# Kernel tuning notes

Hardware: AMD Instinct MI355X
Metric: run time of the kernel (lower is better)

## Reference

```python
import jax, jax.numpy as jnp
import numpy as np

N, M = 4096, 256

def setup_inputs() -> dict:
    key = jax.random.key(0)
    k1, k2 = jax.random.split(key)
    y_pred = jax.random.normal(k1, (N, M), dtype=jnp.float32)
    y = jax.random.normal(k2, (N, 1), dtype=jnp.float32)
    return {"y_pred": y_pred, "y": y}

def reference(y_pred, y):
    n, m = y_pred.shape
    # MAE term: mean(|y_pred - y|), y broadcast over ensemble dim
    mae_loss = jnp.mean(jnp.abs(y_pred - y))
    # Ensemble spread term: sum_{i,k,l} |x[i,k] - x[i,l]| / (n * 2 * m^2)
    # pairwise diffs: [n, m, m]
    pair = jnp.abs(y_pred[:, None, :] - y_pred[:, :, None])
    mix_loss = jnp.sum(pair) / (n * 2 * m ** 2)
    return mae_loss - mix_loss
```

## Files before the change

### kernel.cpp

```cpp
#include <hip/hip_runtime.h>


constexpr int N_ROWS = 4096;
constexpr int M_COLS = 256;
constexpr int ROWS_PER_BLOCK = 4;

__global__ __launch_bounds__(256)
void crps_kernel(const float* __restrict__ y_pred,
                 const float* __restrict__ y,
                 float* __restrict__ out) {
    __shared__ __align__(16) float4 rows[ROWS_PER_BLOCK][M_COLS / 4];
    __shared__ float wsum[ROWS_PER_BLOCK];

    const int wave = threadIdx.x >> 6;
    const int lane = threadIdx.x & 63;
    const int row  = blockIdx.x * ROWS_PER_BLOCK + wave;

    const float4* gp = reinterpret_cast<const float4*>(y_pred + row * M_COLS);
    const float4 xk = gp[lane];
    rows[wave][lane] = xk;
    const float yi = y[row];
    __syncthreads();

    float m0 = 0.0f, m1 = 0.0f, m2 = 0.0f, m3 = 0.0f;
    const float4* r4 = rows[wave];
    #pragma unroll 8
    for (int l = 0; l < M_COLS / 4; ++l) {
        const float4 v = r4[l];
        m0 += fabsf(xk.x - v.x) + fabsf(xk.x - v.y) + fabsf(xk.x - v.z) + fabsf(xk.x - v.w);
        m1 += fabsf(xk.y - v.x) + fabsf(xk.y - v.y) + fabsf(xk.y - v.z) + fabsf(xk.y - v.w);
        m2 += fabsf(xk.z - v.x) + fabsf(xk.z - v.y) + fabsf(xk.z - v.z) + fabsf(xk.z - v.w);
        m3 += fabsf(xk.w - v.x) + fabsf(xk.w - v.y) + fabsf(xk.w - v.z) + fabsf(xk.w - v.w);
    }
    const float mix = (m0 + m1) + (m2 + m3);

    const float mae = fabsf(xk.x - yi) + fabsf(xk.y - yi)
                    + fabsf(xk.z - yi) + fabsf(xk.w - yi);

    constexpr float mae_scale = 1.0f / ((float)N_ROWS * (float)M_COLS);
    constexpr float mix_scale = 1.0f / (2.0f * (float)N_ROWS * (float)M_COLS * (float)M_COLS);
    float part = mae * mae_scale - mix * mix_scale;

    #pragma unroll
    for (int off = 32; off > 0; off >>= 1)
        part += __shfl_down(part, off, 64);

    if (lane == 0) wsum[wave] = part;
    __syncthreads();
    if (threadIdx.x == 0) {
        atomicAdd(out, (wsum[0] + wsum[1]) + (wsum[2] + wsum[3]));
    }
}

extern "C" void kernel_launch(void* const* d_in, const int* in_sizes, int n_in,
                              void* d_out, int out_size, void* d_ws, size_t ws_size,
                              hipStream_t stream) {
    const float* y_pred = (const float*)d_in[0];
    const float* y      = (const float*)d_in[1];
    float* out          = (float*)d_out;

    hipMemsetAsync(out, 0, sizeof(float), stream);

    crps_kernel<<<N_ROWS / ROWS_PER_BLOCK, 256, 0, stream>>>(y_pred, y, out);
}
```

Baseline: 76.33 us.

## Halve-wave per row with 8 values per lane and two-stage deterministic reduction

Each wave now handles two rows, with each half-wave owning one row and each lane holding 8 elements instead of 4. This doubles arithmetic per shared-memory load, so LDS traffic per operation drops and the block count halves. The global atomicAdd and memset are replaced by per-block partials written to workspace and summed by a second single-block kernel. A software-prefetched LDS read and padded rows are added. The costs are an extra kernel launch and higher register use per thread. The __syncthreads between the shared-memory writes and the reads was removed. This relies on each half-wave reading only data written by its own wave.

```diff
diff --git a/kernel.cpp b/kernel.cpp
--- a/kernel.cpp
+++ b/kernel.cpp
@@ -3,39 +3,58 @@
 
 constexpr int N_ROWS = 4096;
 constexpr int M_COLS = 256;
-constexpr int ROWS_PER_BLOCK = 4;
+constexpr int ROWS_PER_BLOCK = 8;
+constexpr int NUM_BLOCKS = N_ROWS / ROWS_PER_BLOCK;
 
 __global__ __launch_bounds__(256)
-void crps_kernel(const float* __restrict__ y_pred,
-                 const float* __restrict__ y,
-                 float* __restrict__ out) {
-    __shared__ __align__(16) float4 rows[ROWS_PER_BLOCK][M_COLS / 4];
-    __shared__ float wsum[ROWS_PER_BLOCK];
+void crps_partial(const float* __restrict__ y_pred,
+                  const float* __restrict__ y,
+                  float* __restrict__ partial) {
+    __shared__ __align__(16) float4 rows[ROWS_PER_BLOCK][M_COLS / 4 + 1];
+    __shared__ float wsum[4];
 
     const int wave = threadIdx.x >> 6;
     const int lane = threadIdx.x & 63;
-    const int row  = blockIdx.x * ROWS_PER_BLOCK + wave;
+    const int half = lane >> 5;
+    const int ll   = lane & 31;
+    const int lrow = wave * 2 + half;
+    const int row  = blockIdx.x * ROWS_PER_BLOCK + lrow;
 
     const float4* gp = reinterpret_cast<const float4*>(y_pred + row * M_COLS);
-    const float4 xk = gp[lane];
-    rows[wave][lane] = xk;
+    const float4 xa = gp[2 * ll];
+    const float4 xb = gp[2 * ll + 1];
+    rows[lrow][2 * ll]     = xa;
+    rows[lrow][2 * ll + 1] = xb;
     const float yi = y[row];
-    __syncthreads();
 
-    float m0 = 0.0f, m1 = 0.0f, m2 = 0.0f, m3 = 0.0f;
-    const float4* r4 = rows[wave];
-    #pragma unroll 8
-    for (int l = 0; l < M_COLS / 4; ++l) {
-        const float4 v = r4[l];
-        m0 += fabsf(xk.x - v.x) + fabsf(xk.x - v.y) + fabsf(xk.x - v.z) + fabsf(xk.x - v.w);
-        m1 += fabsf(xk.y - v.x) + fabsf(xk.y - v.y) + fabsf(xk.y - v.z) + fabsf(xk.y - v.w);
-        m2 += fabsf(xk.z - v.x) + fabsf(xk.z - v.y) + fabsf(xk.z - v.z) + fabsf(xk.z - v.w);
-        m3 += fabsf(xk.w - v.x) + fabsf(xk.w - v.y) + fabsf(xk.w - v.z) + fabsf(xk.w - v.w);
+    float xo[8] = {xa.x, xa.y, xa.z, xa.w, xb.x, xb.y, xb.z, xb.w};
+    float m[8]  = {0, 0, 0, 0, 0, 0, 0, 0};
+
+    const float4* r4 = rows[lrow];
+
+    auto acc = [&](const float4 v) {
+        #pragma unroll
+        for (int j = 0; j < 8; ++j) {
+            m[j] += fabsf(xo[j] - v.x) + fabsf(xo[j] - v.y)
+                  + fabsf(xo[j] - v.z) + fabsf(xo[j] - v.w);
+        }
+    };
+
+    float4 cur = r4[0];
+    #pragma unroll 4
+    for (int l = 0; l < M_COLS / 4 - 1; ++l) {
+        const float4 nxt = r4[l + 1];
+        acc(cur);
+        cur = nxt;
     }
-    const float mix = (m0 + m1) + (m2 + m3);
+    acc(cur);
 
-    const float mae = fabsf(xk.x - yi) + fabsf(xk.y - yi)
-                    + fabsf(xk.z - yi) + fabsf(xk.w - yi);
+    float mix = 0.0f, mae = 0.0f;
+    #pragma unroll
+    for (int j = 0; j < 8; ++j) {
+        mix += m[j];
+        mae += fabsf(xo[j] - yi);
+    }
 
     constexpr float mae_scale = 1.0f / ((float)N_ROWS * (float)M_COLS);
     constexpr float mix_scale = 1.0f / (2.0f * (float)N_ROWS * (float)M_COLS * (float)M_COLS);
@@ -47,8 +66,25 @@
 
     if (lane == 0) wsum[wave] = part;
     __syncthreads();
-    if (threadIdx.x == 0) {
-        atomicAdd(out, (wsum[0] + wsum[1]) + (wsum[2] + wsum[3]));
+    if (threadIdx.x == 0)
+        partial[blockIdx.x] = (wsum[0] + wsum[1]) + (wsum[2] + wsum[3]);
+}
+
+__global__ __launch_bounds__(512)
+void crps_final(const float* __restrict__ partial, float* __restrict__ out) {
+    __shared__ float wsum[8];
+    const int t = threadIdx.x;
+    float v = partial[t];
+    #pragma unroll
+    for (int off = 32; off > 0; off >>= 1)
+        v += __shfl_down(v, off, 64);
+    if ((t & 63) == 0) wsum[t >> 6] = v;
+    __syncthreads();
+    if (t == 0) {
+        float s = 0.0f;
+        #pragma unroll
+        for (int i = 0; i < 8; ++i) s += wsum[i];
+        *out = s;
     }
 }
 
@@ -58,8 +94,8 @@
     const float* y_pred = (const float*)d_in[0];
     const float* y      = (const float*)d_in[1];
     float* out          = (float*)d_out;
+    float* ws           = (float*)d_ws;
 
-    hipMemsetAsync(out, 0, sizeof(float), stream);
-
-    crps_kernel<<<N_ROWS / ROWS_PER_BLOCK, 256, 0, stream>>>(y_pred, y, out);
+    crps_partial<<<NUM_BLOCKS, 256, 0, stream>>>(y_pred, y, ws);
+    crps_final<<<1, 512, 0, stream>>>(ws, out);
 }
```

Measured after the change: 74.30 us. 1.03x faster.

## Fuse abs-add via inline asm, pipeline LDS reads, use two-stage reduction

Applied to the files above, without the earlier changes.

The pairwise inner loop now issues `v_add_f32` with an absolute-value source modifier through inline asm, so each pair term costs a subtract plus a fused abs-add. The next float4 is software-prefetched from LDS while the current one is accumulated. The block barrier before the loop is dropped, since each wave reads only the row it wrote itself. The memset plus 1024 same-address atomicAdds is replaced by a per-block partial buffer in workspace and a second single-block reduction kernel. This trades atomic contention for an extra kernel launch, and the inline asm may block some compiler scheduling.

```diff
diff --git a/kernel.cpp b/kernel.cpp
--- a/kernel.cpp
+++ b/kernel.cpp
@@ -4,11 +4,17 @@
 constexpr int N_ROWS = 4096;
 constexpr int M_COLS = 256;
 constexpr int ROWS_PER_BLOCK = 4;
+constexpr int NUM_BLOCKS = N_ROWS / ROWS_PER_BLOCK;
+
+__device__ __forceinline__ void abs_acc(float& m, float a, float b) {
+    float t = a - b;
+    asm("v_add_f32 %0, %0, |%1|" : "+v"(m) : "v"(t));
+}
 
 __global__ __launch_bounds__(256)
-void crps_kernel(const float* __restrict__ y_pred,
-                 const float* __restrict__ y,
-                 float* __restrict__ out) {
+void crps_partial(const float* __restrict__ y_pred,
+                  const float* __restrict__ y,
+                  float* __restrict__ partial) {
     __shared__ __align__(16) float4 rows[ROWS_PER_BLOCK][M_COLS / 4];
     __shared__ float wsum[ROWS_PER_BLOCK];
 
@@ -20,22 +26,34 @@
     const float4 xk = gp[lane];
     rows[wave][lane] = xk;
     const float yi = y[row];
-    __syncthreads();
 
-    float m0 = 0.0f, m1 = 0.0f, m2 = 0.0f, m3 = 0.0f;
+    const float xo[4] = {xk.x, xk.y, xk.z, xk.w};
+    float m[4] = {0, 0, 0, 0};
+
     const float4* r4 = rows[wave];
-    #pragma unroll 8
-    for (int l = 0; l < M_COLS / 4; ++l) {
-        const float4 v = r4[l];
-        m0 += fabsf(xk.x - v.x) + fabsf(xk.x - v.y) + fabsf(xk.x - v.z) + fabsf(xk.x - v.w);
-        m1 += fabsf(xk.y - v.x) + fabsf(xk.y - v.y) + fabsf(xk.y - v.z) + fabsf(xk.y - v.w);
-        m2 += fabsf(xk.z - v.x) + fabsf(xk.z - v.y) + fabsf(xk.z - v.z) + fabsf(xk.z - v.w);
-        m3 += fabsf(xk.w - v.x) + fabsf(xk.w - v.y) + fabsf(xk.w - v.z) + fabsf(xk.w - v.w);
+
+    auto acc4 = [&](const float4 v) {
+        #pragma unroll
+        for (int j = 0; j < 4; ++j) {
+            abs_acc(m[j], xo[j], v.x);
+            abs_acc(m[j], xo[j], v.y);
+            abs_acc(m[j], xo[j], v.z);
+            abs_acc(m[j], xo[j], v.w);
+        }
+    };
+
+    float4 cur = r4[0];
+    #pragma unroll 4
+    for (int l = 0; l < M_COLS / 4 - 1; ++l) {
+        const float4 nxt = r4[l + 1];
+        acc4(cur);
+        cur = nxt;
     }
-    const float mix = (m0 + m1) + (m2 + m3);
+    acc4(cur);
 
-    const float mae = fabsf(xk.x - yi) + fabsf(xk.y - yi)
-                    + fabsf(xk.z - yi) + fabsf(xk.w - yi);
+    const float mix = (m[0] + m[1]) + (m[2] + m[3]);
+    const float mae = fabsf(xo[0] - yi) + fabsf(xo[1] - yi)
+                    + fabsf(xo[2] - yi) + fabsf(xo[3] - yi);
 
     constexpr float mae_scale = 1.0f / ((float)N_ROWS * (float)M_COLS);
     constexpr float mix_scale = 1.0f / (2.0f * (float)N_ROWS * (float)M_COLS * (float)M_COLS);
@@ -47,9 +65,23 @@
 
     if (lane == 0) wsum[wave] = part;
     __syncthreads();
-    if (threadIdx.x == 0) {
-        atomicAdd(out, (wsum[0] + wsum[1]) + (wsum[2] + wsum[3]));
-    }
+    if (threadIdx.x == 0)
+        partial[blockIdx.x] = (wsum[0] + wsum[1]) + (wsum[2] + wsum[3]);
+}
+
+__global__ __launch_bounds__(256)
+void crps_final(const float* __restrict__ partial, float* __restrict__ out) {
+    __shared__ float wsum[4];
+    const int t = threadIdx.x;
+    const float4 v4 = reinterpret_cast<const float4*>(partial)[t];
+    float v = (v4.x + v4.y) + (v4.z + v4.w);
+    #pragma unroll
+    for (int off = 32; off > 0; off >>= 1)
+        v += __shfl_down(v, off, 64);
+    if ((t & 63) == 0) wsum[t >> 6] = v;
+    __syncthreads();
+    if (t == 0)
+        *out = (wsum[0] + wsum[1]) + (wsum[2] + wsum[3]);
 }
 
 extern "C" void kernel_launch(void* const* d_in, const int* in_sizes, int n_in,
@@ -58,8 +90,8 @@
     const float* y_pred = (const float*)d_in[0];
     const float* y      = (const float*)d_in[1];
     float* out          = (float*)d_out;
+    float* ws           = (float*)d_ws;
 
-    hipMemsetAsync(out, 0, sizeof(float), stream);
-
-    crps_kernel<<<N_ROWS / ROWS_PER_BLOCK, 256, 0, stream>>>(y_pred, y, out);
+    crps_partial<<<NUM_BLOCKS, 256, 0, stream>>>(y_pred, y, ws);
+    crps_final<<<1, 256, 0, stream>>>(ws, out);
 }
```

New measurement: 65.30 us. 14.4% less time.

## Replace O(m^2) pairwise abs-diff sum with per-row bitonic sort and weighted sum

Applied to the files above, without the earlier changes.

The kernel now sorts each row of 256 values inside a wave with a register and shuffle-based bitonic network, then computes the pairwise absolute-difference sum as a rank-weighted linear sum of the sorted values. This removes the quadratic shared-memory loop and the shared row buffer along with its block barrier. In exchange it adds many cross-lane shuffles and min/max steps, and it can round differently from the direct pairwise sum.

```diff
diff --git a/kernel.cpp b/kernel.cpp
--- a/kernel.cpp
+++ b/kernel.cpp
@@ -4,42 +4,76 @@
 constexpr int N_ROWS = 4096;
 constexpr int M_COLS = 256;
 constexpr int ROWS_PER_BLOCK = 4;
+constexpr int NUM_BLOCKS = N_ROWS / ROWS_PER_BLOCK;
+
+__device__ __forceinline__ void ce_dir(float& a, float& b, bool up) {
+    const float lo = fminf(a, b);
+    const float hi = fmaxf(a, b);
+    a = up ? lo : hi;
+    b = up ? hi : lo;
+}
+
+__device__ __forceinline__ void ce_x(float v[4], int xmask, bool keepmin) {
+    #pragma unroll
+    for (int r = 0; r < 4; ++r) {
+        const float w  = __shfl_xor(v[r], xmask, 64);
+        const float mn = fminf(v[r], w);
+        const float mx = fmaxf(v[r], w);
+        v[r] = keepmin ? mn : mx;
+    }
+}
+
+template <int K>
+__device__ __forceinline__ void bitonic_merge(float v[4], int lane, bool up) {
+    #pragma unroll
+    for (int j = K / 2; j >= 4; j >>= 1) {
+        const bool keepmin = (up == ((lane & (j >> 2)) == 0));
+        ce_x(v, j >> 2, keepmin);
+    }
+    ce_dir(v[0], v[2], up);
+    ce_dir(v[1], v[3], up);
+    ce_dir(v[0], v[1], up);
+    ce_dir(v[2], v[3], up);
+}
 
 __global__ __launch_bounds__(256)
 void crps_kernel(const float* __restrict__ y_pred,
                  const float* __restrict__ y,
                  float* __restrict__ out) {
-    __shared__ __align__(16) float4 rows[ROWS_PER_BLOCK][M_COLS / 4];
     __shared__ float wsum[ROWS_PER_BLOCK];
 
     const int wave = threadIdx.x >> 6;
     const int lane = threadIdx.x & 63;
     const int row  = blockIdx.x * ROWS_PER_BLOCK + wave;
 
-    const float4* gp = reinterpret_cast<const float4*>(y_pred + row * M_COLS);
-    const float4 xk = gp[lane];
-    rows[wave][lane] = xk;
+    const float4 xk = reinterpret_cast<const float4*>(y_pred + row * M_COLS)[lane];
     const float yi = y[row];
-    __syncthreads();
 
-    float m0 = 0.0f, m1 = 0.0f, m2 = 0.0f, m3 = 0.0f;
-    const float4* r4 = rows[wave];
-    #pragma unroll 8
-    for (int l = 0; l < M_COLS / 4; ++l) {
-        const float4 v = r4[l];
-        m0 += fabsf(xk.x - v.x) + fabsf(xk.x - v.y) + fabsf(xk.x - v.z) + fabsf(xk.x - v.w);
-        m1 += fabsf(xk.y - v.x) + fabsf(xk.y - v.y) + fabsf(xk.y - v.z) + fabsf(xk.y - v.w);
-        m2 += fabsf(xk.z - v.x) + fabsf(xk.z - v.y) + fabsf(xk.z - v.z) + fabsf(xk.z - v.w);
-        m3 += fabsf(xk.w - v.x) + fabsf(xk.w - v.y) + fabsf(xk.w - v.z) + fabsf(xk.w - v.w);
-    }
-    const float mix = (m0 + m1) + (m2 + m3);
+    float v[4] = {xk.x, xk.y, xk.z, xk.w};
 
-    const float mae = fabsf(xk.x - yi) + fabsf(xk.y - yi)
-                    + fabsf(xk.z - yi) + fabsf(xk.w - yi);
+    const float mae = fabsf(v[0] - yi) + fabsf(v[1] - yi)
+                    + fabsf(v[2] - yi) + fabsf(v[3] - yi);
+
+    ce_dir(v[0], v[1], true);
+    ce_dir(v[2], v[3], false);
+    bitonic_merge<4>(v, lane, (lane & 1) == 0);
+    bitonic_merge<8>(v, lane, (lane & 2) == 0);
+    bitonic_merge<16>(v, lane, (lane & 4) == 0);
+    bitonic_merge<32>(v, lane, (lane & 8) == 0);
+    bitonic_merge<64>(v, lane, (lane & 16) == 0);
+    bitonic_merge<128>(v, lane, (lane & 32) == 0);
+    bitonic_merge<256>(v, lane, true);
+
+    const float base = (float)(8 * lane + 1 - M_COLS);
+    float rm = 0.0f;
+    rm = fmaf(v[0], base + 0.0f, rm);
+    rm = fmaf(v[1], base + 2.0f, rm);
+    rm = fmaf(v[2], base + 4.0f, rm);
+    rm = fmaf(v[3], base + 6.0f, rm);
 
     constexpr float mae_scale = 1.0f / ((float)N_ROWS * (float)M_COLS);
-    constexpr float mix_scale = 1.0f / (2.0f * (float)N_ROWS * (float)M_COLS * (float)M_COLS);
-    float part = mae * mae_scale - mix * mix_scale;
+    constexpr float mix_scale = 1.0f / ((float)N_ROWS * (float)M_COLS * (float)M_COLS);
+    float part = mae * mae_scale - rm * mix_scale;
 
     #pragma unroll
     for (int off = 32; off > 0; off >>= 1)
@@ -47,9 +81,8 @@
 
     if (lane == 0) wsum[wave] = part;
     __syncthreads();
-    if (threadIdx.x == 0) {
+    if (threadIdx.x == 0)
         atomicAdd(out, (wsum[0] + wsum[1]) + (wsum[2] + wsum[3]));
-    }
 }
 
 extern "C" void kernel_launch(void* const* d_in, const int* in_sizes, int n_in,
@@ -61,5 +94,5 @@
 
     hipMemsetAsync(out, 0, sizeof(float), stream);
 
-    crps_kernel<<<N_ROWS / ROWS_PER_BLOCK, 256, 0, stream>>>(y_pred, y, out);
+    crps_kernel<<<NUM_BLOCKS, 256, 0, stream>>>(y_pred, y, out);
 }
```

Result: faster. 71.90 us (-5.8%).
